# Kernel optimization log

Measured on AMD Instinct MI355X. Metric: run time of the kernel, lower is better.

## Reference

```python
import jax, jax.numpy as jnp
import numpy as np

GN_EPS = 1e-5
NN_EPS = 1e-8


def _three_nn_interpolate(xyz1, xyz2, points2):
    # xyz1: (B,N,3), xyz2: (B,M,3), points2: (B,M,C) -> (B,N,C)
    src_sq = jnp.sum(xyz1 ** 2, axis=-1, keepdims=True)          # (B,N,1)
    dst_sq = jnp.sum(xyz2 ** 2, axis=-1)[:, None, :]             # (B,1,M)
    inner = jnp.einsum('bnd,bmd->bnm', xyz1, xyz2)               # (B,N,M)
    dist = src_sq - 2.0 * inner + dst_sq                         # (B,N,M)
    neg_d, idx = jax.lax.top_k(-dist, 3)                         # (B,N,3)
    d = -neg_d
    inv = 1.0 / (d + NN_EPS)
    w = inv / jnp.sum(inv, axis=-1, keepdims=True)               # (B,N,3)
    grouped = jax.vmap(lambda p, i: p[i])(points2, idx)          # (B,N,3,C)
    return jnp.sum(grouped * w[..., None], axis=2)               # (B,N,C)


def _group_norm(x, weight, bias, groups):
    # x: (B,C,N)
    B, C, N = x.shape
    xg = x.reshape(B, groups, C // groups, N)
    mu = jnp.mean(xg, axis=(2, 3), keepdims=True)
    var = jnp.var(xg, axis=(2, 3), keepdims=True)
    xg = (xg - mu) * jax.lax.rsqrt(var + GN_EPS)
    x = xg.reshape(B, C, N)
    return x * weight[None, :, None] + bias[None, :, None]


def setup_inputs() -> dict:
    key = jax.random.key(0)
    ks = jax.random.split(key, 10)
    B, N, M, C1, C2 = 8, 8192, 2048, 128, 256
    mlp = [256, 128]
    in_ch = C1 + C2
    inp = {
        'xyz1': jax.random.normal(ks[0], (B, N, 3), dtype=jnp.float32),
        'xyz2': jax.random.normal(ks[1], (B, M, 3), dtype=jnp.float32),
        'points1': jax.random.normal(ks[2], (B, N, C1), dtype=jnp.float32),
        'points2': jax.random.normal(ks[3], (B, M, C2), dtype=jnp.float32),
        'w0': jax.random.normal(ks[4], (mlp[0], in_ch), dtype=jnp.float32) * (1.0 / np.sqrt(in_ch)),
        'w1': jax.random.normal(ks[5], (mlp[1], mlp[0]), dtype=jnp.float32) * (1.0 / np.sqrt(mlp[0])),
        'gn0_w': jnp.ones((mlp[0],), dtype=jnp.float32),
        'gn0_b': jnp.zeros((mlp[0],), dtype=jnp.float32),
        'gn1_w': jnp.ones((mlp[1],), dtype=jnp.float32),
        'gn1_b': jnp.zeros((mlp[1],), dtype=jnp.float32),
    }
    return inp


def reference(xyz1, xyz2, points1, points2, w0, w1, gn0_w, gn0_b, gn1_w, gn1_b):
    interpolated = _three_nn_interpolate(xyz1, xyz2, points2)    # (B,N,C2)
    feat = jnp.concatenate([points1, interpolated], axis=-1)     # (B,N,C1+C2)
    # conv1d kernel size 1 == pointwise matmul; work in (B,C,N) layout for GN
    h = jnp.einsum('bnc,oc->bon', feat, w0)                      # (B,256,N)
    h = jax.nn.relu(_group_norm(h, gn0_w, gn0_b, groups=min(32, w0.shape[0])))
    h = jnp.einsum('bcn,oc->bon', h, w1)                         # (B,128,N)
    h = jax.nn.relu(_group_norm(h, gn1_w, gn1_b, groups=min(32, w1.shape[0])))
    return jnp.transpose(h, (0, 2, 1))                           # (B,N,128)
```

## Files before the change

### kernel.cpp

```cpp
#include <hip/hip_runtime.h>


#define DEVI __device__ __forceinline__

static constexpr int B  = 8;
static constexpr int N  = 8192;
static constexpr int M  = 2048;
static constexpr int C1 = 128;
static constexpr int C2 = 256;
static constexpr int CIN = C1 + C2;
static constexpr int H0 = 256;
static constexpr int H1 = 128;
static constexpr int BN = B * N;
static constexpr int NSEG = 8;
static constexpr int SEGL = M / NSEG;

typedef __bf16 bf16x8 __attribute__((ext_vector_type(8)));
typedef float  f32x4  __attribute__((ext_vector_type(4)));
typedef unsigned short ushort8v __attribute__((ext_vector_type(8)));

DEVI float bf2f(unsigned short u) {
    union { unsigned int i; float f; } v; v.i = ((unsigned int)u) << 16; return v.f;
}
DEVI unsigned short f2bf(float f) {
    union { float f; unsigned int i; } v; v.f = f;
    unsigned int x = v.i;
    return (unsigned short)((x + 0x7fffu + ((x >> 16) & 1u)) >> 16);
}
DEVI float ldin(const void* p, size_t i, int bf) {
    return bf ? bf2f(((const unsigned short*)p)[i]) : ((const float*)p)[i];
}
DEVI void ld8(const void* p, size_t i, int bf, float r[8]) {
    if (bf) {
        const ushort8v u = *(const ushort8v*)((const unsigned short*)p + i);
#pragma unroll
        for (int k = 0; k < 8; k++) r[k] = bf2f(u[k]);
    } else {
        const float4 a = *(const float4*)((const float*)p + i);
        const float4 b = *(const float4*)((const float*)p + i + 4);
        r[0] = a.x; r[1] = a.y; r[2] = a.z; r[3] = a.w;
        r[4] = b.x; r[5] = b.y; r[6] = b.z; r[7] = b.w;
    }
}
DEVI void ld8b(const unsigned short* p, size_t i, float r[8]) {
    const ushort8v u = *(const ushort8v*)(p + i);
#pragma unroll
    for (int k = 0; k < 8; k++) r[k] = bf2f(u[k]);
}

DEVI void gload16(const void* g, void* l) {
    __builtin_amdgcn_global_load_lds(
        (const __attribute__((address_space(1))) void*)g,
        (__attribute__((address_space(3))) void*)l, 16, 0, 0);
}

__global__ __launch_bounds__(64) void detect_dtype_kernel(const void* __restrict__ xyz1,
                                                          int* __restrict__ flag)
{
    const unsigned short* u = (const unsigned short*)xyz1;
    const int lane = threadIdx.x;
    const float av = fabsf(bf2f(u[2 * lane]));
    const bool in_range = (av >= 1e-4f && av <= 100.0f);
    const unsigned long long m = __ballot(in_range);
    if (lane == 0) flag[0] = (__popcll(m) >= 32) ? 1 : 0;
}

DEVI void cvt8(const void* src, unsigned short* dst, size_t j8, int bf) {
    if (bf) {
        *(ushort8v*)(dst + j8 * 8) = *(const ushort8v*)((const unsigned short*)src + j8 * 8);
    } else {
        float r[8];
        ld8(src, j8 * 8, 0, r);
        ushort8v o;
#pragma unroll
        for (int k = 0; k < 8; k++) o[k] = f2bf(r[k]);
        *(ushort8v*)(dst + j8 * 8) = o;
    }
}

__global__ __launch_bounds__(256) void prep_kernel(
    const void* __restrict__ w0, const void* __restrict__ w1,
    const void* __restrict__ p1, const void* __restrict__ p2,
    const void* __restrict__ xyz2,
    unsigned short* __restrict__ w0b, unsigned short* __restrict__ w1b,
    unsigned short* __restrict__ pb1, unsigned short* __restrict__ pb2,
    float4* __restrict__ c4, float* __restrict__ partz,
    const int* __restrict__ flag)
{
    const int bf = flag[0];
    constexpr int R0 = H0 * CIN / 8;
    constexpr int R1 = H1 * H0 / 8;
    constexpr int R2 = B * M;
    constexpr int R3 = BN * C1 / 8;
    constexpr int R4 = B * M * C2 / 8;
    constexpr int R5 = 1024;
    constexpr int TOT = R0 + R1 + R2 + R3 + R4 + R5;
    for (int i = blockIdx.x * blockDim.x + threadIdx.x; i < TOT; i += gridDim.x * blockDim.x) {
        int j = i;
        if (j < R0) { cvt8(w0, w0b, j, bf); continue; }
        j -= R0;
        if (j < R1) { cvt8(w1, w1b, j, bf); continue; }
        j -= R1;
        if (j < R2) {
            const float x = ldin(xyz2, (size_t)j * 3 + 0, bf);
            const float y = ldin(xyz2, (size_t)j * 3 + 1, bf);
            const float z = ldin(xyz2, (size_t)j * 3 + 2, bf);
            const float sq = __fadd_rn(__fadd_rn(__fmul_rn(x, x), __fmul_rn(y, y)), __fmul_rn(z, z));
            c4[j] = make_float4(x, y, z, 0.5f * sq);
            continue;
        }
        j -= R2;
        if (j < R3) { cvt8(p1, pb1, j, bf); continue; }
        j -= R3;
        if (j < R4) { cvt8(p2, pb2, j, bf); continue; }
        j -= R4;
        partz[j] = 0.f;
    }
}

__global__ __launch_bounds__(256) void knn3_split_kernel(
    const void* __restrict__ xyz1, const float4* __restrict__ c4,
    int* __restrict__ ci, const int* __restrict__ flag)
{
    const int bf = flag[0];
    const int tid = threadIdx.x;
    const int gid = blockIdx.x * 256 + tid;
    const int s = blockIdx.y;
    const int b = __builtin_amdgcn_readfirstlane(gid >> 13);

    const float x1 = ldin(xyz1, (size_t)gid * 3 + 0, bf);
    const float y1 = ldin(xyz1, (size_t)gid * 3 + 1, bf);
    const float z1 = ldin(xyz1, (size_t)gid * 3 + 2, bf);

    const float4* __restrict__ cand = c4 + b * M + s * SEGL;
    const int jbase = s * SEGL;
    constexpr int HALF = SEGL / 2;

    float a0 = 3.4e38f, a1 = 3.4e38f, a2 = 3.4e38f;
    int   ia0 = 0, ia1 = 0, ia2 = 0;
    float g0 = 3.4e38f, g1 = 3.4e38f, g2 = 3.4e38f;
    int   ig0 = 0, ig1 = 0, ig2 = 0;

#pragma unroll 4
    for (int j = 0; j < HALF; ++j) {
        const float4 pA = cand[j];
        const float4 pB = cand[j + HALF];
        const float sA = __builtin_fmaf(-x1, pA.x,
                          __builtin_fmaf(-y1, pA.y,
                           __builtin_fmaf(-z1, pA.z, pA.w)));
        const float sB = __builtin_fmaf(-x1, pB.x,
                          __builtin_fmaf(-y1, pB.y,
                           __builtin_fmaf(-z1, pB.z, pB.w)));
        {
            const int jn = jbase + j;
            const bool c0 = sA < a0;
            const float t1 = fmaxf(sA, a0); a0 = fminf(sA, a0);
            const int  tj1 = c0 ? ia0 : jn; ia0 = c0 ? jn : ia0;
            const bool c1 = t1 < a1;
            const float t2 = fmaxf(t1, a1); a1 = fminf(t1, a1);
            const int  tj2 = c1 ? ia1 : tj1; ia1 = c1 ? tj1 : ia1;
            const bool c2 = t2 < a2;
            a2 = fminf(t2, a2); ia2 = c2 ? tj2 : ia2;
        }
        {
            const int jn = jbase + HALF + j;
            const bool c0 = sB < g0;
            const float t1 = fmaxf(sB, g0); g0 = fminf(sB, g0);
            const int  tj1 = c0 ? ig0 : jn; ig0 = c0 ? jn : ig0;
            const bool c1 = t1 < g1;
            const float t2 = fmaxf(t1, g1); g1 = fminf(t1, g1);
            const int  tj2 = c1 ? ig1 : tj1; ig1 = c1 ? tj1 : ig1;
            const bool c2 = t2 < g2;
            g2 = fminf(t2, g2); ig2 = c2 ? tj2 : ig2;
        }
    }

    float mv[3] = { g0, g1, g2 };
    int   mi[3] = { ig0, ig1, ig2 };
#pragma unroll
    for (int k = 0; k < 3; ++k) {
        const float sv = mv[k]; const int jn = mi[k];
        const bool c0 = sv < a0;
        const float t1 = fmaxf(sv, a0); a0 = fminf(sv, a0);
        const int  tj1 = c0 ? ia0 : jn; ia0 = c0 ? jn : ia0;
        const bool c1 = t1 < a1;
        const float t2 = fmaxf(t1, a1); a1 = fminf(t1, a1);
        const int  tj2 = c1 ? ia1 : tj1; ia1 = c1 ? tj1 : ia1;
        const bool c2 = t2 < a2;
        a2 = fminf(t2, a2); ia2 = c2 ? tj2 : ia2;
    }

    ci[(size_t)(s * 3 + 0) * BN + gid] = ia0;
    ci[(size_t)(s * 3 + 1) * BN + gid] = ia1;
    ci[(size_t)(s * 3 + 2) * BN + gid] = ia2;
}

__global__ __launch_bounds__(256) void knn3_merge_kernel(
    const void* __restrict__ xyz1, const float4* __restrict__ c4,
    const int* __restrict__ ci,
    int* __restrict__ nn_idx, float* __restrict__ nn_w,
    const int* __restrict__ flag)
{
    const int bf = flag[0];
    const int gid = blockIdx.x * 256 + threadIdx.x;
    const int b = gid >> 13;

    const float x1 = ldin(xyz1, (size_t)gid * 3 + 0, bf);
    const float y1 = ldin(xyz1, (size_t)gid * 3 + 1, bf);
    const float z1 = ldin(xyz1, (size_t)gid * 3 + 2, bf);
    const float sq1 = __fadd_rn(__fadd_rn(__fmul_rn(x1, x1), __fmul_rn(y1, y1)), __fmul_rn(z1, z1));

    float bd0 = 3.4e38f, bd1 = 3.4e38f, bd2 = 3.4e38f;
    int   bi0 = 0x7fffffff, bi1 = 0x7fffffff, bi2 = 0x7fffffff;

#pragma unroll
    for (int k = 0; k < 3 * NSEG; ++k) {
        const int ix = ci[(size_t)k * BN + gid];
        const float4 p = c4[b * M + ix];
        const float inner = __fadd_rn(__fadd_rn(__fmul_rn(x1, p.x), __fmul_rn(y1, p.y)),
                                      __fmul_rn(z1, p.z));
        const float pw2 = p.w + p.w;
        const float d = __fadd_rn(__fsub_rn(sq1, __fmul_rn(2.0f, inner)), pw2);
        const bool lt2 = (d < bd2) || (d == bd2 && ix < bi2);
        if (lt2) {
            const bool lt0 = (d < bd0) || (d == bd0 && ix < bi0);
            const bool lt1 = (d < bd1) || (d == bd1 && ix < bi1);
            if (lt0)      { bd2 = bd1; bi2 = bi1; bd1 = bd0; bi1 = bi0; bd0 = d; bi0 = ix; }
            else if (lt1) { bd2 = bd1; bi2 = bi1; bd1 = d; bi1 = ix; }
            else          { bd2 = d; bi2 = ix; }
        }
    }

    const float v0 = 1.0f / (bd0 + 1e-8f);
    const float v1 = 1.0f / (bd1 + 1e-8f);
    const float v2 = 1.0f / (bd2 + 1e-8f);
    const float s = v0 + v1 + v2;
    nn_idx[gid * 3 + 0] = bi0; nn_idx[gid * 3 + 1] = bi1; nn_idx[gid * 3 + 2] = bi2;
    nn_w[gid * 3 + 0] = v0 / s; nn_w[gid * 3 + 1] = v1 / s; nn_w[gid * 3 + 2] = v2 / s;
}

__global__ __launch_bounds__(256) void interp_concat_kernel(
    const unsigned short* __restrict__ pb1, const unsigned short* __restrict__ pb2,
    const int* __restrict__ nn_idx, const float* __restrict__ nn_w,
    unsigned short* __restrict__ feat)
{
    const int total = BN * (CIN / 8);
    for (int idx = blockIdx.x * blockDim.x + threadIdx.x; idx < total; idx += gridDim.x * blockDim.x) {
        const int c8 = idx % 48;
        const int p  = idx / 48;
        const int c  = c8 * 8;
        if (c < C1) {
            *(ushort8v*)(feat + (size_t)idx * 8) =
                *(const ushort8v*)(pb1 + (size_t)p * C1 + c);
        } else {
            const int b  = p >> 13;
            const int c2 = c - C1;
            const int*   id = nn_idx + p * 3;
            const float* wv = nn_w  + p * 3;
            float t0[8], t1[8], t2[8];
            ld8b(pb2, (size_t)(b * M + id[0]) * C2 + c2, t0);
            ld8b(pb2, (size_t)(b * M + id[1]) * C2 + c2, t1);
            ld8b(pb2, (size_t)(b * M + id[2]) * C2 + c2, t2);
            const float w0v = wv[0], w1v = wv[1], w2v = wv[2];
            ushort8v o;
#pragma unroll
            for (int k = 0; k < 8; k++)
                o[k] = f2bf(w0v * t0[k] + w1v * t1[k] + w2v * t2[k]);
            *(ushort8v*)(feat + (size_t)idx * 8) = o;
        }
    }
}

__global__ __launch_bounds__(512) void gemm1_kernel(
    const unsigned short* __restrict__ A,
    const unsigned short* __restrict__ W,
    unsigned short* __restrict__ h0, float2* __restrict__ part)
{
    constexpr int K = CIN;
    constexpr int COUT = H0;
    __shared__ __align__(16) char lds[49152];

    const int tid = threadIdx.x;
    const int l   = tid & 63;
    const int w   = tid >> 6;
    const int rowBase = blockIdx.x * 128;
    const int b = rowBase >> 13;

    const int srow  = l >> 3;
    const int sslot = l & 7;

    f32x4 acc[4][4];
#pragma unroll
    for (int i = 0; i < 4; i++)
#pragma unroll
        for (int j = 0; j < 4; j++) acc[i][j] = (f32x4)0.0f;

    const int wr  = w >> 2;
    const int wc  = w & 3;
    const int rl  = l & 15;
    const int kq  = l >> 4;
    const int swz = (l & 7) << 4;
    int aoff[4], boff[4];
#pragma unroll
    for (int i = 0; i < 4; i++) {
        aoff[i] = (wr * 64 + i * 16 + rl) * 128;
        boff[i] = 16384 + (wc * 64 + i * 16 + rl) * 128;
    }

    constexpr int NT = K / 64;

#pragma unroll 1
    for (int t = 0; t < NT; ++t) {
        const int k0 = t * 64;
#pragma unroll
        for (int i = 0; i < 6; ++i) {
            const int ch = w * 6 + i;
            if (ch < 16) {
                const int r  = ch * 8 + srow;
                const int ke = (sslot ^ (r & 7)) << 3;
                gload16(A + ((size_t)(rowBase + r) * K + k0 + ke), lds + ch * 1024);
            } else {
                const int rb = (ch - 16) * 8 + srow;
                const int ke = (sslot ^ (rb & 7)) << 3;
                gload16(W + ((size_t)rb * K + k0 + ke), lds + 16384 + (ch - 16) * 1024);
            }
        }
        __syncthreads();
#pragma unroll
        for (int ks = 0; ks < 2; ++ks) {
            const int kb = (ks * 64 + kq * 16) ^ swz;
            bf16x8 af[4], bfr[4];
#pragma unroll
            for (int i = 0; i < 4; i++) af[i]  = *(const bf16x8*)(lds + aoff[i] + kb);
#pragma unroll
            for (int j = 0; j < 4; j++) bfr[j] = *(const bf16x8*)(lds + boff[j] + kb);
#pragma unroll
            for (int i = 0; i < 4; i++)
#pragma unroll
                for (int j = 0; j < 4; j++)
                    acc[i][j] = __builtin_amdgcn_mfma_f32_16x16x32_bf16(af[i], bfr[j], acc[i][j], 0, 0, 0);
        }
        __syncthreads();
    }

    const int crow = rowBase + wr * 64 + kq * 4;
    const int ccol = wc * 64 + rl;
    float gsum[4], gss[4];
#pragma unroll
    for (int j = 0; j < 4; j++) {
        float s = 0.f, ss = 0.f;
#pragma unroll
        for (int i = 0; i < 4; i++)
#pragma unroll
            for (int r = 0; r < 4; r++) {
                const unsigned short hb = f2bf(acc[i][j][r]);
                h0[(size_t)(crow + i * 16 + r) * COUT + ccol + j * 16] = hb;
                const float x = bf2f(hb);
                s += x; ss += x * x;
            }
        gsum[j] = s; gss[j] = ss;
    }
    __syncthreads();
    float2* sred = (float2*)lds;
    if (tid < 32) sred[tid] = make_float2(0.f, 0.f);
    __syncthreads();
#pragma unroll
    for (int j = 0; j < 4; j++) {
        const int g = wc * 8 + j * 2 + (rl >> 3);
        atomicAdd(&sred[g].x, gsum[j]);
        atomicAdd(&sred[g].y, gss[j]);
    }
    __syncthreads();
    if (tid < 32) {
        atomicAdd(&part[b * 32 + tid].x, sred[tid].x);
        atomicAdd(&part[b * 32 + tid].y, sred[tid].y);
    }
}

__global__ __launch_bounds__(256) void gemm2_kernel(
    const unsigned short* __restrict__ h0, const float2* __restrict__ st0,
    const void* __restrict__ gw, const void* __restrict__ gb,
    const unsigned short* __restrict__ W,
    unsigned short* __restrict__ h1, float2* __restrict__ part,
    const int* __restrict__ flag)
{
    constexpr int K = H0;
    constexpr int COUT = H1;
    __shared__ __align__(16) char lds[32768];

    const int bf = flag[0];
    const int tid = threadIdx.x;
    const int l   = tid & 63;
    const int w   = tid >> 6;
    const int rowBase = blockIdx.x * 128;
    const int b = rowBase >> 13;

    const int srow  = l >> 3;
    const int sslot = l & 7;

    f32x4 acc[4][4];
#pragma unroll
    for (int i = 0; i < 4; i++)
#pragma unroll
        for (int j = 0; j < 4; j++) acc[i][j] = (f32x4)0.0f;

    const int wr  = (tid >> 7) & 1;
    const int wc  = (tid >> 6) & 1;
    const int rl  = l & 15;
    const int kq  = l >> 4;
    const int swz = (l & 7) << 4;
    int aoff[4], boff[4];
#pragma unroll
    for (int i = 0; i < 4; i++) {
        aoff[i] = (wr * 64 + i * 16 + rl) * 128;
        boff[i] = 16384 + (wc * 64 + i * 16 + rl) * 128;
    }

    constexpr int NT = K / 64;

#pragma unroll 1
    for (int t = 0; t < NT; ++t) {
        const int k0 = t * 64;
#pragma unroll
        for (int i = 0; i < 4; ++i) {
            const int cb = w * 4 + i;
            const int r  = cb * 8 + srow;
            const int ke = (sslot ^ (r & 7)) << 3;
            gload16(W + ((size_t)r * K + k0 + ke), lds + 16384 + cb * 1024);
        }
#pragma unroll
        for (int i = 0; i < 4; ++i) {
            const int r = (w * 4 + i) * 8 + srow;
            const int kslot = sslot ^ (r & 7);
            const int c = k0 + (kslot << 3);
            const float2 ms = st0[b * 32 + (c >> 3)];
            float gwv[8], gbv[8];
            ld8(gw, c, bf, gwv);
            ld8(gb, c, bf, gbv);
            const ushort8v hv = *(const ushort8v*)(h0 + (size_t)(rowBase + r) * H0 + c);
            ushort8v o;
#pragma unroll
            for (int k = 0; k < 8; k++) {
                const float x = bf2f(hv[k]);
                o[k] = f2bf(fmaxf((x - ms.x) * ms.y * gwv[k] + gbv[k], 0.f));
            }
            *(ushort8v*)(lds + r * 128 + (sslot << 4)) = o;
        }
        __syncthreads();
#pragma unroll
        for (int ks = 0; ks < 2; ++ks) {
            const int kb = (ks * 64 + kq * 16) ^ swz;
            bf16x8 af[4], bfr[4];
#pragma unroll
            for (int i = 0; i < 4; i++) af[i]  = *(const bf16x8*)(lds + aoff[i] + kb);
#pragma unroll
            for (int j = 0; j < 4; j++) bfr[j] = *(const bf16x8*)(lds + boff[j] + kb);
#pragma unroll
            for (int i = 0; i < 4; i++)
#pragma unroll
                for (int j = 0; j < 4; j++)
                    acc[i][j] = __builtin_amdgcn_mfma_f32_16x16x32_bf16(af[i], bfr[j], acc[i][j], 0, 0, 0);
        }
        __syncthreads();
    }

    const int crow = rowBase + wr * 64 + kq * 4;
    const int ccol = wc * 64 + rl;
    float gsum[4], gss[4];
#pragma unroll
    for (int j = 0; j < 4; j++) {
        float s = 0.f, ss = 0.f;
#pragma unroll
        for (int i = 0; i < 4; i++)
#pragma unroll
            for (int r = 0; r < 4; r++) {
                const unsigned short hb = f2bf(acc[i][j][r]);
                h1[(size_t)(crow + i * 16 + r) * COUT + ccol + j * 16] = hb;
                const float x = bf2f(hb);
                s += x; ss += x * x;
            }
        gsum[j] = s; gss[j] = ss;
    }
    __syncthreads();
    float2* sred = (float2*)lds;
    if (tid < 32) sred[tid] = make_float2(0.f, 0.f);
    __syncthreads();
#pragma unroll
    for (int j = 0; j < 4; j++) {
        const int g = wc * 16 + j * 4 + (rl >> 2);
        atomicAdd(&sred[g].x, gsum[j]);
        atomicAdd(&sred[g].y, gss[j]);
    }
    __syncthreads();
    if (tid < 32) {
        atomicAdd(&part[b * 32 + tid].x, sred[tid].x);
        atomicAdd(&part[b * 32 + tid].y, sred[tid].y);
    }
}

__global__ __launch_bounds__(256) void gn_finalize_kernel(
    const float2* __restrict__ part, float2* __restrict__ st, float cnt)
{
    const int t = threadIdx.x;
    const float2 p = part[t];
    const float mu  = p.x / cnt;
    const float var = p.y / cnt - mu * mu;
    st[t] = make_float2(mu, rsqrtf(var + 1e-5f));
}

__global__ __launch_bounds__(256) void gn_norm_relu_kernel(
    const unsigned short* __restrict__ h, const float2* __restrict__ st,
    const void* __restrict__ gw, const void* __restrict__ gb,
    void* __restrict__ out, int C, int cpg, int total4,
    const int* __restrict__ flag)
{
    const int bf = flag[0];
    const int C4 = C >> 2;
    for (int i4 = blockIdx.x * blockDim.x + threadIdx.x; i4 < total4; i4 += gridDim.x * blockDim.x) {
        const int c = (i4 % C4) * 4;
        const int p = i4 / C4;
        const int b = p >> 13;
        const float2 ms = st[b * (C / cpg) + c / cpg];
        const ushort4 hv = *(const ushort4*)(h + (size_t)i4 * 4);
        float r[4] = { bf2f(hv.x), bf2f(hv.y), bf2f(hv.z), bf2f(hv.w) };
#pragma unroll
        for (int k = 0; k < 4; k++) {
            const float gwv = ldin(gw, c + k, bf);
            const float gbv = ldin(gb, c + k, bf);
            r[k] = fmaxf((r[k] - ms.x) * ms.y * gwv + gbv, 0.f);
        }
        if (bf) {
            ushort4 o;
            o.x = f2bf(r[0]); o.y = f2bf(r[1]); o.z = f2bf(r[2]); o.w = f2bf(r[3]);
            *(ushort4*)((unsigned short*)out + (size_t)i4 * 4) = o;
        } else {
            float4 o; o.x = r[0]; o.y = r[1]; o.z = r[2]; o.w = r[3];
            *(float4*)((float*)out + (size_t)i4 * 4) = o;
        }
    }
}

extern "C" void kernel_launch(void* const* d_in, const int* in_sizes, int n_in,
                              void* d_out, int out_size, void* d_ws, size_t ws_size,
                              hipStream_t stream)
{
    const void* xyz1    = d_in[0];
    const void* xyz2    = d_in[1];
    const void* points1 = d_in[2];
    const void* points2 = d_in[3];
    const void* w0      = d_in[4];
    const void* w1      = d_in[5];
    const void* gn0w    = d_in[6];
    const void* gn0b    = d_in[7];
    const void* gn1w    = d_in[8];
    const void* gn1b    = d_in[9];

    char* ws = (char*)d_ws;
    int*            nn_idx = (int*)ws;
    float*          nn_w   = (float*)(ws + 786432);
    unsigned short* feat   = (unsigned short*)(ws + 1572864);
    unsigned short* h1     = feat;
    unsigned short* h0     = (unsigned short*)(ws + 51904512);
    unsigned short* w0b    = (unsigned short*)(ws + 85458944);
    unsigned short* w1b    = (unsigned short*)(ws + 85655552);
    unsigned short* pb1    = (unsigned short*)(ws + 85721088);
    unsigned short* pb2    = (unsigned short*)(ws + 102498304);
    float4*         c4     = (float4*)(ws + 110886912);
    int*            ci     = (int*)(ws + 111149056);
    float2*         part0  = (float2*)(ws + 117440512);
    float2*         part1  = (float2*)(ws + 117442560);
    float2*         st0    = (float2*)(ws + 117444608);
    float2*         st1    = (float2*)(ws + 117446656);
    int*            flag   = (int*)(ws + 117448704);

    detect_dtype_kernel<<<1, 64, 0, stream>>>(xyz1, flag);

    prep_kernel<<<2048, 256, 0, stream>>>(w0, w1, points1, points2, xyz2,
                                          w0b, w1b, pb1, pb2, c4, (float*)part0, flag);

    {
        dim3 g(BN / 256, NSEG);
        knn3_split_kernel<<<g, 256, 0, stream>>>(xyz1, c4, ci, flag);
    }
    knn3_merge_kernel<<<BN / 256, 256, 0, stream>>>(xyz1, c4, ci, nn_idx, nn_w, flag);

    interp_concat_kernel<<<2048, 256, 0, stream>>>(pb1, pb2, nn_idx, nn_w, feat);

    gemm1_kernel<<<BN / 128, 512, 0, stream>>>(feat, w0b, h0, part0);
    gn_finalize_kernel<<<1, 256, 0, stream>>>(part0, st0, (float)N * (H0 / 32));

    gemm2_kernel<<<BN / 128, 256, 0, stream>>>(h0, st0, gn0w, gn0b, w1b, h1, part1, flag);
    gn_finalize_kernel<<<1, 256, 0, stream>>>(part1, st1, (float)N * (H1 / 32));

    gn_norm_relu_kernel<<<1024, 256, 0, stream>>>(h1, st1, gn1w, gn1b, d_out,
                                                  H1, H1 / 32, BN * H1 / 4, flag);
}
```

Baseline: 303.9 us.

## Fuse knn merge with interpolation/concat, drop points1 prep copy and GN finalize kernels

Merges the kNN merge and the interpolate-concat into one kernel that keeps neighbor indices and weights in shared memory, and converts points1 directly into feat instead of staging a bf16 copy in prep. The two single-block GroupNorm finalize launches are removed, and each consumer block recomputes mean and rstd from the partial sums into LDS. This cuts launches and global round trips of nn_idx, nn_w and pb1. In exchange, half the threads idle during the merge phase and the stats are recomputed redundantly in every block.

Result: slower. 316.3 us (+4.1%).

```diff
diff --git a/kernel.cpp b/kernel.cpp
--- a/kernel.cpp
+++ b/kernel.cpp
@@ -80,10 +80,9 @@
 
 __global__ __launch_bounds__(256) void prep_kernel(
     const void* __restrict__ w0, const void* __restrict__ w1,
-    const void* __restrict__ p1, const void* __restrict__ p2,
-    const void* __restrict__ xyz2,
+    const void* __restrict__ p2, const void* __restrict__ xyz2,
     unsigned short* __restrict__ w0b, unsigned short* __restrict__ w1b,
-    unsigned short* __restrict__ pb1, unsigned short* __restrict__ pb2,
+    unsigned short* __restrict__ pb2,
     float4* __restrict__ c4, float* __restrict__ partz,
     const int* __restrict__ flag)
 {
@@ -91,10 +90,9 @@
     constexpr int R0 = H0 * CIN / 8;
     constexpr int R1 = H1 * H0 / 8;
     constexpr int R2 = B * M;
-    constexpr int R3 = BN * C1 / 8;
     constexpr int R4 = B * M * C2 / 8;
     constexpr int R5 = 1024;
-    constexpr int TOT = R0 + R1 + R2 + R3 + R4 + R5;
+    constexpr int TOT = R0 + R1 + R2 + R4 + R5;
     for (int i = blockIdx.x * blockDim.x + threadIdx.x; i < TOT; i += gridDim.x * blockDim.x) {
         int j = i;
         if (j < R0) { cvt8(w0, w0b, j, bf); continue; }
@@ -110,8 +108,6 @@
             continue;
         }
         j -= R2;
-        if (j < R3) { cvt8(p1, pb1, j, bf); continue; }
-        j -= R3;
         if (j < R4) { cvt8(p2, pb2, j, bf); continue; }
         j -= R4;
         partz[j] = 0.f;
@@ -195,79 +191,86 @@
     ci[(size_t)(s * 3 + 2) * BN + gid] = ia2;
 }
 
-__global__ __launch_bounds__(256) void knn3_merge_kernel(
+__global__ __launch_bounds__(256) void interp_merge_kernel(
+    const void* __restrict__ p1, const unsigned short* __restrict__ pb2,
     const void* __restrict__ xyz1, const float4* __restrict__ c4,
     const int* __restrict__ ci,
-    int* __restrict__ nn_idx, float* __restrict__ nn_w,
-    const int* __restrict__ flag)
-{
+    unsigned short* __restrict__ feat, const int* __restrict__ flag)
+{
+    __shared__ int   sidx[128][3];
+    __shared__ float sw[128][3];
+
     const int bf = flag[0];
-    const int gid = blockIdx.x * 256 + threadIdx.x;
-    const int b = gid >> 13;
-
-    const float x1 = ldin(xyz1, (size_t)gid * 3 + 0, bf);
-    const float y1 = ldin(xyz1, (size_t)gid * 3 + 1, bf);
-    const float z1 = ldin(xyz1, (size_t)gid * 3 + 2, bf);
-    const float sq1 = __fadd_rn(__fadd_rn(__fmul_rn(x1, x1), __fmul_rn(y1, y1)), __fmul_rn(z1, z1));
-
-    float bd0 = 3.4e38f, bd1 = 3.4e38f, bd2 = 3.4e38f;
-    int   bi0 = 0x7fffffff, bi1 = 0x7fffffff, bi2 = 0x7fffffff;
-
-#pragma unroll
-    for (int k = 0; k < 3 * NSEG; ++k) {
-        const int ix = ci[(size_t)k * BN + gid];
-        const float4 p = c4[b * M + ix];
-        const float inner = __fadd_rn(__fadd_rn(__fmul_rn(x1, p.x), __fmul_rn(y1, p.y)),
-                                      __fmul_rn(z1, p.z));
-        const float pw2 = p.w + p.w;
-        const float d = __fadd_rn(__fsub_rn(sq1, __fmul_rn(2.0f, inner)), pw2);
-        const bool lt2 = (d < bd2) || (d == bd2 && ix < bi2);
-        if (lt2) {
-            const bool lt0 = (d < bd0) || (d == bd0 && ix < bi0);
-            const bool lt1 = (d < bd1) || (d == bd1 && ix < bi1);
-            if (lt0)      { bd2 = bd1; bi2 = bi1; bd1 = bd0; bi1 = bi0; bd0 = d; bi0 = ix; }
-            else if (lt1) { bd2 = bd1; bi2 = bi1; bd1 = d; bi1 = ix; }
-            else          { bd2 = d; bi2 = ix; }
-        }
-    }
-
-    const float v0 = 1.0f / (bd0 + 1e-8f);
-    const float v1 = 1.0f / (bd1 + 1e-8f);
-    const float v2 = 1.0f / (bd2 + 1e-8f);
-    const float s = v0 + v1 + v2;
-    nn_idx[gid * 3 + 0] = bi0; nn_idx[gid * 3 + 1] = bi1; nn_idx[gid * 3 + 2] = bi2;
-    nn_w[gid * 3 + 0] = v0 / s; nn_w[gid * 3 + 1] = v1 / s; nn_w[gid * 3 + 2] = v2 / s;
-}
-
-__global__ __launch_bounds__(256) void interp_concat_kernel(
-    const unsigned short* __restrict__ pb1, const unsigned short* __restrict__ pb2,
-    const int* __restrict__ nn_idx, const float* __restrict__ nn_w,
-    unsigned short* __restrict__ feat)
-{
-    const int total = BN * (CIN / 8);
-    for (int idx = blockIdx.x * blockDim.x + threadIdx.x; idx < total; idx += gridDim.x * blockDim.x) {
-        const int c8 = idx % 48;
-        const int p  = idx / 48;
+    const int t = threadIdx.x;
+    const int qbase = blockIdx.x * 128;
+    const int b = qbase >> 13;
+
+    if (t < 128) {
+        const int q = qbase + t;
+        const float x1 = ldin(xyz1, (size_t)q * 3 + 0, bf);
+        const float y1 = ldin(xyz1, (size_t)q * 3 + 1, bf);
+        const float z1 = ldin(xyz1, (size_t)q * 3 + 2, bf);
+        const float sq1 = __fadd_rn(__fadd_rn(__fmul_rn(x1, x1), __fmul_rn(y1, y1)), __fmul_rn(z1, z1));
+
+        float bd0 = 3.4e38f, bd1 = 3.4e38f, bd2 = 3.4e38f;
+        int   bi0 = 0x7fffffff, bi1 = 0x7fffffff, bi2 = 0x7fffffff;
+
+#pragma unroll
+        for (int k = 0; k < 3 * NSEG; ++k) {
+            const int ix = ci[(size_t)k * BN + q];
+            const float4 p = c4[b * M + ix];
+            const float inner = __fadd_rn(__fadd_rn(__fmul_rn(x1, p.x), __fmul_rn(y1, p.y)),
+                                          __fmul_rn(z1, p.z));
+            const float pw2 = p.w + p.w;
+            const float d = __fadd_rn(__fsub_rn(sq1, __fmul_rn(2.0f, inner)), pw2);
+            const bool lt2 = (d < bd2) || (d == bd2 && ix < bi2);
+            if (lt2) {
+                const bool lt0 = (d < bd0) || (d == bd0 && ix < bi0);
+                const bool lt1 = (d < bd1) || (d == bd1 && ix < bi1);
+                if (lt0)      { bd2 = bd1; bi2 = bi1; bd1 = bd0; bi1 = bi0; bd0 = d; bi0 = ix; }
+                else if (lt1) { bd2 = bd1; bi2 = bi1; bd1 = d; bi1 = ix; }
+                else          { bd2 = d; bi2 = ix; }
+            }
+        }
+
+        const float v0 = 1.0f / (bd0 + 1e-8f);
+        const float v1 = 1.0f / (bd1 + 1e-8f);
+        const float v2 = 1.0f / (bd2 + 1e-8f);
+        const float s = v0 + v1 + v2;
+        sidx[t][0] = bi0; sidx[t][1] = bi1; sidx[t][2] = bi2;
+        sw[t][0] = v0 / s; sw[t][1] = v1 / s; sw[t][2] = v2 / s;
+    }
+    __syncthreads();
+
+#pragma unroll 1
+    for (int it = 0; it < 24; ++it) {
+        const int tt = it * 256 + t;
+        const int ql = tt / 48;
+        const int c8 = tt % 48;
         const int c  = c8 * 8;
+        const int q  = qbase + ql;
+        ushort8v o;
         if (c < C1) {
-            *(ushort8v*)(feat + (size_t)idx * 8) =
-                *(const ushort8v*)(pb1 + (size_t)p * C1 + c);
+            if (bf) {
+                o = *(const ushort8v*)((const unsigned short*)p1 + (size_t)q * C1 + c);
+            } else {
+                float r[8];
+                ld8(p1, (size_t)q * C1 + c, 0, r);
+#pragma unroll
+                for (int k = 0; k < 8; k++) o[k] = f2bf(r[k]);
+            }
         } else {
-            const int b  = p >> 13;
             const int c2 = c - C1;
-            const int*   id = nn_idx + p * 3;
-            const float* wv = nn_w  + p * 3;
             float t0[8], t1[8], t2[8];
-            ld8b(pb2, (size_t)(b * M + id[0]) * C2 + c2, t0);
-            ld8b(pb2, (size_t)(b * M + id[1]) * C2 + c2, t1);
-            ld8b(pb2, (size_t)(b * M + id[2]) * C2 + c2, t2);
-            const float w0v = wv[0], w1v = wv[1], w2v = wv[2];
-            ushort8v o;
+            ld8b(pb2, (size_t)(b * M + sidx[ql][0]) * C2 + c2, t0);
+            ld8b(pb2, (size_t)(b * M + sidx[ql][1]) * C2 + c2, t1);
+            ld8b(pb2, (size_t)(b * M + sidx[ql][2]) * C2 + c2, t2);
+            const float w0v = sw[ql][0], w1v = sw[ql][1], w2v = sw[ql][2];
 #pragma unroll
             for (int k = 0; k < 8; k++)
                 o[k] = f2bf(w0v * t0[k] + w1v * t1[k] + w2v * t2[k]);
-            *(ushort8v*)(feat + (size_t)idx * 8) = o;
-        }
+        }
+        *(ushort8v*)(feat + (size_t)q * CIN + c) = o;
     }
 }
 
@@ -378,15 +381,16 @@
 }
 
 __global__ __launch_bounds__(256) void gemm2_kernel(
-    const unsigned short* __restrict__ h0, const float2* __restrict__ st0,
+    const unsigned short* __restrict__ h0, const float2* __restrict__ part0,
     const void* __restrict__ gw, const void* __restrict__ gb,
     const unsigned short* __restrict__ W,
-    unsigned short* __restrict__ h1, float2* __restrict__ part,
+    unsigned short* __restrict__ h1, float2* __restrict__ part1,
     const int* __restrict__ flag)
 {
     constexpr int K = H0;
     constexpr int COUT = H1;
     __shared__ __align__(16) char lds[32768];
+    __shared__ float2 stlds[32];
 
     const int bf = flag[0];
     const int tid = threadIdx.x;
@@ -395,6 +399,15 @@
     const int rowBase = blockIdx.x * 128;
     const int b = rowBase >> 13;
 
+    if (tid < 32) {
+        const float2 p = part0[b * 32 + tid];
+        const float cnt = (float)N * 8.0f;
+        const float mu  = p.x / cnt;
+        const float var = p.y / cnt - mu * mu;
+        stlds[tid] = make_float2(mu, rsqrtf(var + 1e-5f));
+    }
+    __syncthreads();
+
     const int srow  = l >> 3;
     const int sslot = l & 7;
 
@@ -433,7 +446,7 @@
             const int r = (w * 4 + i) * 8 + srow;
             const int kslot = sslot ^ (r & 7);
             const int c = k0 + (kslot << 3);
-            const float2 ms = st0[b * 32 + (c >> 3)];
+            const float2 ms = stlds[c >> 3];
             float gwv[8], gbv[8];
             ld8(gw, c, bf, gwv);
             ld8(gb, c, bf, gbv);
@@ -493,34 +506,37 @@
     }
     __syncthreads();
     if (tid < 32) {
-        atomicAdd(&part[b * 32 + tid].x, sred[tid].x);
-        atomicAdd(&part[b * 32 + tid].y, sred[tid].y);
-    }
-}
-
-__global__ __launch_bounds__(256) void gn_finalize_kernel(
-    const float2* __restrict__ part, float2* __restrict__ st, float cnt)
-{
-    const int t = threadIdx.x;
-    const float2 p = part[t];
-    const float mu  = p.x / cnt;
-    const float var = p.y / cnt - mu * mu;
-    st[t] = make_float2(mu, rsqrtf(var + 1e-5f));
+        atomicAdd(&part1[b * 32 + tid].x, sred[tid].x);
+        atomicAdd(&part1[b * 32 + tid].y, sred[tid].y);
+    }
 }
 
 __global__ __launch_bounds__(256) void gn_norm_relu_kernel(
-    const unsigned short* __restrict__ h, const float2* __restrict__ st,
+    const unsigned short* __restrict__ h, const float2* __restrict__ part1,
     const void* __restrict__ gw, const void* __restrict__ gb,
-    void* __restrict__ out, int C, int cpg, int total4,
-    const int* __restrict__ flag)
-{
+    void* __restrict__ out, const int* __restrict__ flag)
+{
+    constexpr int C = H1;
+    constexpr int cpg = 4;
+    constexpr int C4 = C >> 2;
+    constexpr int total4 = BN * C / 4;
+
+    __shared__ float2 stlds[256];
+    {
+        const float2 p = part1[threadIdx.x];
+        const float cnt = (float)N * (float)cpg;
+        const float mu  = p.x / cnt;
+        const float var = p.y / cnt - mu * mu;
+        stlds[threadIdx.x] = make_float2(mu, rsqrtf(var + 1e-5f));
+    }
+    __syncthreads();
+
     const int bf = flag[0];
-    const int C4 = C >> 2;
     for (int i4 = blockIdx.x * blockDim.x + threadIdx.x; i4 < total4; i4 += gridDim.x * blockDim.x) {
         const int c = (i4 % C4) * 4;
         const int p = i4 / C4;
         const int b = p >> 13;
-        const float2 ms = st[b * (C / cpg) + c / cpg];
+        const float2 ms = stlds[b * 32 + c / cpg];
         const ushort4 hv = *(const ushort4*)(h + (size_t)i4 * 4);
         float r[4] = { bf2f(hv.x), bf2f(hv.y), bf2f(hv.z), bf2f(hv.w) };
 #pragma unroll
@@ -556,42 +572,35 @@
     const void* gn1b    = d_in[9];
 
     char* ws = (char*)d_ws;
-    int*            nn_idx = (int*)ws;
-    float*          nn_w   = (float*)(ws + 786432);
-    unsigned short* feat   = (unsigned short*)(ws + 1572864);
+    unsigned short* feat   = (unsigned short*)ws;
     unsigned short* h1     = feat;
-    unsigned short* h0     = (unsigned short*)(ws + 51904512);
-    unsigned short* w0b    = (unsigned short*)(ws + 85458944);
-    unsigned short* w1b    = (unsigned short*)(ws + 85655552);
-    unsigned short* pb1    = (unsigned short*)(ws + 85721088);
-    unsigned short* pb2    = (unsigned short*)(ws + 102498304);
-    float4*         c4     = (float4*)(ws + 110886912);
-    int*            ci     = (int*)(ws + 111149056);
-    float2*         part0  = (float2*)(ws + 117440512);
-    float2*         part1  = (float2*)(ws + 117442560);
-    float2*         st0    = (float2*)(ws + 117444608);
-    float2*         st1    = (float2*)(ws + 117446656);
-    int*            flag   = (int*)(ws + 117448704);
+    unsigned short* h0     = (unsigned short*)(ws + 50331648);
+    unsigned short* w0b    = (unsigned short*)(ws + 83886080);
+    unsigned short* w1b    = (unsigned short*)(ws + 84082688);
+    unsigned short* pb2    = (unsigned short*)(ws + 84148224);
+    float4*         c4     = (float4*)(ws + 92536832);
+    int*            ci     = (int*)(ws + 92798976);
+    float2*         part0  = (float2*)(ws + 99090432);
+    float2*         part1  = (float2*)(ws + 99092480);
+    int*            flag   = (int*)(ws + 99094528);
 
     detect_dtype_kernel<<<1, 64, 0, stream>>>(xyz1, flag);
 
-    prep_kernel<<<2048, 256, 0, stream>>>(w0, w1, points1, points2, xyz2,
-                                          w0b, w1b, pb1, pb2, c4, (float*)part0, flag);
+    prep_kernel<<<1024, 256, 0, stream>>>(w0, w1, points2, xyz2,
+                                          w0b, w1b, pb2, c4, (float*)part0, flag);
 
     {
         dim3 g(BN / 256, NSEG);
         knn3_split_kernel<<<g, 256, 0, stream>>>(xyz1, c4, ci, flag);
     }
-    knn3_merge_kernel<<<BN / 256, 256, 0, stream>>>(xyz1, c4, ci, nn_idx, nn_w, flag);
-
-    interp_concat_kernel<<<2048, 256, 0, stream>>>(pb1, pb2, nn_idx, nn_w, feat);
+
+    interp_merge_kernel<<<BN / 128, 256, 0, stream>>>(points1, pb2, xyz1, c4, ci,
+                                                      feat, flag);
 
     gemm1_kernel<<<BN / 128, 512, 0, stream>>>(feat, w0b, h0, part0);
-    gn_finalize_kernel<<<1, 256, 0, stream>>>(part0, st0, (float)N * (H0 / 32));
-
-    gemm2_kernel<<<BN / 128, 256, 0, stream>>>(h0, st0, gn0w, gn0b, w1b, h1, part1, flag);
-    gn_finalize_kernel<<<1, 256, 0, stream>>>(part1, st1, (float)N * (H1 / 32));
-
-    gn_norm_relu_kernel<<<1024, 256, 0, stream>>>(h1, st1, gn1w, gn1b, d_out,
-                                                  H1, H1 / 32, BN * H1 / 4, flag);
-}
+
+    gemm2_kernel<<<BN / 128, 256, 0, stream>>>(h0, part0, gn0w, gn0b, w1b, h1,
+                                               part1, flag);
+
+    gn_norm_relu_kernel<<<1024, 256, 0, stream>>>(h1, part1, gn1w, gn1b, d_out, flag);
+}
```
